# Optimization experiments

Hardware: AMD Instinct MI355X
Metric: run time of the kernel (lower is better)

The kernel has to match this reference:

```python
import jax, jax.numpy as jnp
import numpy as np

INPUT_SIZE = 768
HIDDEN = [512, 256, 128]
LATENT = 32
NUM_LEVELS = 3
CODEBOOK_SIZE = 256
BATCH = 131072


def _init_linear(key, d_in, d_out):
    kw, kb = jax.random.split(key)
    lim = 1.0 / np.sqrt(d_in)
    W = jax.random.uniform(kw, (d_in, d_out), jnp.float32, -lim, lim)
    b = jax.random.uniform(kb, (d_out,), jnp.float32, -lim, lim)
    return W, b


def setup_inputs() -> dict:
    key = jax.random.key(0)
    keys = jax.random.split(key, 16)
    inp = {"x": jax.random.normal(keys[0], (BATCH, INPUT_SIZE), jnp.float32)}
    enc_dims = [INPUT_SIZE] + HIDDEN + [LATENT]          # 768->512->256->128->32
    dec_dims = [LATENT] + HIDDEN[::-1] + [INPUT_SIZE]     # 32->128->256->512->768
    for i in range(4):
        W, b = _init_linear(keys[1 + i], enc_dims[i], enc_dims[i + 1])
        inp[f"enc_W{i}"], inp[f"enc_b{i}"] = W, b
        W, b = _init_linear(keys[6 + i], dec_dims[i], dec_dims[i + 1])
        inp[f"dec_W{i}"], inp[f"dec_b{i}"] = W, b
    inp["codebooks"] = jax.random.normal(keys[12], (NUM_LEVELS, CODEBOOK_SIZE, LATENT), jnp.float32)
    return inp


def _mlp(x, Ws, bs):
    # Linear -> ReLU (-> Dropout p=0, identity) between layers, final layer linear.
    n = len(Ws)
    for i in range(n):
        x = x @ Ws[i] + bs[i]
        if i < n - 1:
            x = jax.nn.relu(x)
    return x


def _quantize(z, codebooks):
    # Residual vector quantization over NUM_LEVELS codebooks.
    L, K, D = codebooks.shape
    r = z
    idxs, rs, es = [], [], []
    for l in range(L):
        c = codebooks[l]                                  # [K, D]
        # squared-distance argmin (same argmin as cdist)
        d = jnp.sum(r * r, axis=-1, keepdims=True) - 2.0 * (r @ c.T) + jnp.sum(c * c, axis=-1)
        idx = jnp.argmin(d, axis=-1)                      # [B]
        e = c[idx]                                        # [B, D] gather
        idxs.append(idx)
        rs.append(r)
        es.append(e)
        r = r - e
    quantized = jnp.stack(idxs, axis=1)                   # [B, L] int codes
    r_stack = jnp.stack(rs, axis=1)                       # [B, L, D] residual inputs per level
    e_stack = jnp.stack(es, axis=1)                       # [B, L, D] selected embeddings
    sum_e = jnp.sum(e_stack, axis=1)                      # [B, D]
    # straight-through estimator
    z_hat = z + jax.lax.stop_gradient(sum_e - z)
    counts = jnp.sum(jax.nn.one_hot(quantized, K, dtype=jnp.float32), axis=0)  # [L, K] usage
    return quantized, r_stack, e_stack, z_hat, counts


def reference(x,
              enc_W0, enc_b0, enc_W1, enc_b1, enc_W2, enc_b2, enc_W3, enc_b3,
              dec_W0, dec_b0, dec_W1, dec_b1, dec_W2, dec_b2, dec_W3, dec_b3,
              codebooks):
    encoded = _mlp(x, [enc_W0, enc_W1, enc_W2, enc_W3], [enc_b0, enc_b1, enc_b2, enc_b3])
    quantized, r, e, z_hat, counts = _quantize(encoded, codebooks)
    decoded = _mlp(z_hat, [dec_W0, dec_W1, dec_W2, dec_W3], [dec_b0, dec_b1, dec_b2, dec_b3])
    return decoded, r, e, counts, quantized
```

## Files before the change

### kernel.cpp

```cpp
#include <hip/hip_runtime.h>
#include <hip/hip_bf16.h>
#include <cfloat>

#define B_TOTAL 131072
#define IN_DIM  768
#define NLEV    3
#define KCODE   256

typedef unsigned short u16;
typedef unsigned int   u32;
typedef __attribute__((ext_vector_type(8))) short bf16x8;
typedef __attribute__((ext_vector_type(4))) float f32x4;

#define GLOAD_LDS(g, l)                                                        \
    __builtin_amdgcn_global_load_lds(                                          \
        (const __attribute__((address_space(1))) u32*)(g),                     \
        (__attribute__((address_space(3))) u32*)(l), 16, 0, 0)

#define SWZ(row) ((((row) >> 1) & 3u) << 4)

__device__ __forceinline__ u16 f2bf(float x) {
    union { __hip_bfloat16 h; u16 u; } c;
    c.h = __float2bfloat16(x);
    return c.u;
}
__device__ __forceinline__ float bf2f(u32 lo16) {
    union { u32 v; float f; } c;
    c.v = lo16 << 16;
    return c.f;
}
__device__ __forceinline__ u32 pack2(float a, float b) {
    return (u32)f2bf(a) | ((u32)f2bf(b) << 16);
}

__device__ __forceinline__ u32 xcd_swizzle(u32 orig, u32 nwg) {
    const u32 xcd = orig & 7u, q8 = nwg >> 3, r8 = nwg & 7u;
    return (xcd < r8 ? xcd * (q8 + 1) : r8 * (q8 + 1) + (xcd - r8) * q8)
           + (orig >> 3);
}

template<int K, int N, bool AF32, bool RELU, bool OUTF32>
__global__ __launch_bounds__(512)
void gemm_mfma(const void* __restrict__ A_, const u16* __restrict__ Wt,
               const float* __restrict__ bias, void* __restrict__ C_)
{
    constexpr int NK  = K / 32;
    constexpr int NCB = N / 128;
    __shared__ u16 As[3][8192];
    __shared__ u16 Bs[3][4096];

    const int tid  = threadIdx.x;
    const int lane = tid & 63;
    const int wid  = tid >> 6;
    const int wrow = wid >> 1;
    const int wcol = wid & 1;

    const u32 wg = xcd_swizzle(blockIdx.x, gridDim.x);
    const int col0 = (int)(wg % NCB) * 128;
    const int row0 = (int)(wg / NCB) * 256;

    const u16*   Ab = (const u16*)A_;
    const float* Af = (const float*)A_;

    f32x4 acc[4][4];
    #pragma unroll
    for (int i = 0; i < 4; ++i)
        #pragma unroll
        for (int j = 0; j < 4; ++j) acc[i][j] = (f32x4){0.f, 0.f, 0.f, 0.f};

    auto stage_B = [&](u16* dstbase, const u16* src) {
        const u32 o   = (u32)(tid * 16);
        const u32 row = o >> 6;
        const u32 cbs = (o & 63u) ^ SWZ(row);
        GLOAD_LDS((const char*)(src + (size_t)row * K) + cbs,
                  dstbase + wid * 512);
    };
    auto stage_A = [&](u16* dstbase, const u16* src) {
        #pragma unroll
        for (int i = 0; i < 2; ++i) {
            const u32 o   = (u32)(i * 8192 + tid * 16);
            const u32 row = o >> 6;
            const u32 cbs = (o & 63u) ^ SWZ(row);
            GLOAD_LDS((const char*)(src + (size_t)row * K) + cbs,
                      dstbase + (i * 4096 + wid * 512));
        }
    };
    auto stage_tile = [&](int buf, int kt) {
        stage_B(&Bs[buf][0], Wt + (size_t)col0 * K + kt * 32);
        stage_A(&As[buf][0], Ab + (size_t)row0 * K + kt * 32);
    };

    auto compute = [&](int buf) {
        const char* Ab8 = (const char*)&As[buf][0];
        const char* Bb8 = (const char*)&Bs[buf][0];
        const int kb = (lane >> 4) * 16;
        bf16x8 af[4], bf[4];
        #pragma unroll
        for (int mf = 0; mf < 4; ++mf) {
            const int r = wrow * 64 + mf * 16 + (lane & 15);
            af[mf] = *(const bf16x8*)(Ab8 + r * 64 + (kb ^ SWZ(r)));
        }
        #pragma unroll
        for (int nf = 0; nf < 4; ++nf) {
            const int r = wcol * 64 + nf * 16 + (lane & 15);
            bf[nf] = *(const bf16x8*)(Bb8 + r * 64 + (kb ^ SWZ(r)));
        }
        __builtin_amdgcn_s_setprio(1);
        #pragma unroll
        for (int mf = 0; mf < 4; ++mf)
            #pragma unroll
            for (int nf = 0; nf < 4; ++nf)
                acc[mf][nf] = __builtin_amdgcn_mfma_f32_16x16x32_bf16(
                    af[mf], bf[nf], acc[mf][nf], 0, 0, 0);
        __builtin_amdgcn_s_setprio(0);
    };

    if constexpr (AF32) {
        float4 fa[4];
        auto loadA = [&](int kt) {
            const int row = tid >> 1;
            const int ce0 = (tid & 1) * 16;
            const float* s = &Af[(size_t)(row0 + row) * K + kt * 32 + ce0];
            fa[0] = *(const float4*)(s + 0);
            fa[1] = *(const float4*)(s + 4);
            fa[2] = *(const float4*)(s + 8);
            fa[3] = *(const float4*)(s + 12);
        };
        auto writeA = [&](int buf) {
            const int row = tid >> 1;
            const u32 cb0 = (u32)((tid & 1) * 32);
            const u32 sw  = SWZ(row);
            char* lb = (char*)&As[buf][0] + row * 64;
            *(uint4*)(lb + ((cb0 + 0) ^ sw)) = make_uint4(
                pack2(fa[0].x, fa[0].y), pack2(fa[0].z, fa[0].w),
                pack2(fa[1].x, fa[1].y), pack2(fa[1].z, fa[1].w));
            *(uint4*)(lb + ((cb0 + 16) ^ sw)) = make_uint4(
                pack2(fa[2].x, fa[2].y), pack2(fa[2].z, fa[2].w),
                pack2(fa[3].x, fa[3].y), pack2(fa[3].z, fa[3].w));
        };

        loadA(0);
        stage_B(&Bs[0][0], Wt + (size_t)col0 * K);
        writeA(0);
        if (NK > 1) {
            loadA(1);
            stage_B(&Bs[1][0], Wt + (size_t)col0 * K + 32);
        }

        #pragma unroll 1
        for (int kt = 0; kt < NK; ++kt) {
            if (kt == NK - 1) asm volatile("s_waitcnt vmcnt(0) lgkmcnt(0)");
            else              asm volatile("s_waitcnt vmcnt(5) lgkmcnt(0)");
            __builtin_amdgcn_sched_barrier(0);
            __builtin_amdgcn_s_barrier();
            __builtin_amdgcn_sched_barrier(0);
            if (kt + 1 < NK) writeA((kt + 1) % 3);
            if (kt + 2 < NK) {
                loadA(kt + 2);
                stage_B(&Bs[(kt + 2) % 3][0],
                        Wt + (size_t)col0 * K + (kt + 2) * 32);
            }
            compute(kt % 3);
        }
    } else {
        stage_tile(0, 0);
        if (NK > 1) stage_tile(1, 1);
        int cb_ = 0, sb_ = 2;
        #pragma unroll 1
        for (int kt = 0; kt < NK; ++kt) {
            if (kt == NK - 1) asm volatile("s_waitcnt vmcnt(0)");
            else              asm volatile("s_waitcnt vmcnt(3)");
            __builtin_amdgcn_sched_barrier(0);
            __builtin_amdgcn_s_barrier();
            __builtin_amdgcn_sched_barrier(0);
            if (kt + 2 < NK) stage_tile(sb_, kt + 2);
            compute(cb_);
            cb_ = (cb_ == 2) ? 0 : cb_ + 1;
            sb_ = (sb_ == 2) ? 0 : sb_ + 1;
        }
    }

    #pragma unroll
    for (int nf = 0; nf < 4; ++nf) {
        const int col = col0 + wcol * 64 + nf * 16 + (lane & 15);
        const float bv = bias[col];
        #pragma unroll
        for (int mf = 0; mf < 4; ++mf) {
            const int rbase = row0 + wrow * 64 + mf * 16 + (lane >> 4) * 4;
            #pragma unroll
            for (int r = 0; r < 4; ++r) {
                float o = acc[mf][nf][r] + bv;
                if (RELU) o = fmaxf(o, 0.f);
                if constexpr (OUTF32)
                    ((float*)C_)[(size_t)(rbase + r) * N + col] = o;
                else
                    ((u16*)C_)[(size_t)(rbase + r) * N + col] = f2bf(o);
            }
        }
    }
}

__global__ __launch_bounds__(256)
void prep(const float* __restrict__ eW0, const float* __restrict__ eW1,
          const float* __restrict__ eW2, const float* __restrict__ dW0,
          const float* __restrict__ dW1, const float* __restrict__ dW2,
          const float* __restrict__ dW3,
          u16* __restrict__ tE0, u16* __restrict__ tE1, u16* __restrict__ tE2,
          u16* __restrict__ tD0, u16* __restrict__ tD1, u16* __restrict__ tD2,
          u16* __restrict__ tD3, u32* __restrict__ ghist)
{
    const int i = blockIdx.x * 256 + threadIdx.x;
    if (i < 393216) {
        const int k = i >> 9, n = i & 511;
        tE0[(size_t)n * 768 + k] = f2bf(eW0[i]);
    } else if (i < 524288) {
        const int j = i - 393216, k = j >> 8, n = j & 255;
        tE1[(size_t)n * 512 + k] = f2bf(eW1[j]);
    } else if (i < 557056) {
        const int j = i - 524288, k = j >> 7, n = j & 127;
        tE2[(size_t)n * 256 + k] = f2bf(eW2[j]);
    } else if (i < 561152) {
        const int j = i - 557056, k = j >> 7, n = j & 127;
        tD0[(size_t)n * 32 + k] = f2bf(dW0[j]);
    } else if (i < 593920) {
        const int j = i - 561152, k = j >> 8, n = j & 255;
        tD1[(size_t)n * 128 + k] = f2bf(dW1[j]);
    } else if (i < 724992) {
        const int j = i - 593920, k = j >> 9, n = j & 511;
        tD2[(size_t)n * 256 + k] = f2bf(dW2[j]);
    } else if (i < 1118208) {
        const int j = i - 724992, k = j / 768, n = j - k * 768;
        tD3[(size_t)n * 512 + k] = f2bf(dW3[j]);
    } else if (i < 1118976) {
        ghist[i - 1118208] = 0;
    }
}

__global__ __launch_bounds__(256)
void vq_kernel(const u16* __restrict__ h3, const float* __restrict__ eW3,
               const float* __restrict__ eb3, const float* __restrict__ cb,
               float* __restrict__ r_out, float* __restrict__ e_out,
               float* __restrict__ q_out, u16* __restrict__ se_ws,
               u32* __restrict__ ghist, size_t grow_base)
{
    __shared__ float W3[128 * 32];
    __shared__ float ebv[32];
    __shared__ float clds[256 * 36];
    __shared__ float cc2[256];
    __shared__ u32   lh[NLEV * KCODE];

    const int tid = threadIdx.x;
    const size_t lrow = (size_t)blockIdx.x * 256 + tid;
    const size_t grow = grow_base + lrow;

    for (int i = tid; i < 128 * 32; i += 256) W3[i] = eW3[i];
    if (tid < 32) ebv[tid] = eb3[tid];
    for (int i = tid; i < NLEV * KCODE; i += 256) lh[i] = 0;
    __syncthreads();

    float r[32];
    #pragma unroll
    for (int j = 0; j < 32; ++j) r[j] = ebv[j];
    {
        const u32* hrow = (const u32*)h3 + lrow * 64;
        #pragma unroll 2
        for (int k2 = 0; k2 < 64; ++k2) {
            const u32 v = hrow[k2];
            const float x0 = bf2f(v & 0xffffu), x1 = bf2f(v >> 16);
            const float* w0 = &W3[(2 * k2) * 32];
            const float* w1 = &W3[(2 * k2 + 1) * 32];
            #pragma unroll
            for (int j4 = 0; j4 < 8; ++j4) {
                const float4 a = *(const float4*)&w0[4 * j4];
                const float4 b = *(const float4*)&w1[4 * j4];
                r[4*j4+0] = fmaf(x1, b.x, fmaf(x0, a.x, r[4*j4+0]));
                r[4*j4+1] = fmaf(x1, b.y, fmaf(x0, a.y, r[4*j4+1]));
                r[4*j4+2] = fmaf(x1, b.z, fmaf(x0, a.z, r[4*j4+2]));
                r[4*j4+3] = fmaf(x1, b.w, fmaf(x0, a.w, r[4*j4+3]));
            }
        }
    }

    float z0[32];
    #pragma unroll
    for (int j = 0; j < 32; ++j) z0[j] = r[j];

    #pragma unroll 1
    for (int l = 0; l < NLEV; ++l) {
        __syncthreads();
        {
            const float* cl = cb + ((size_t)l * KCODE + tid) * 32;
            float s = 0.f;
            #pragma unroll
            for (int m = 0; m < 8; ++m) {
                const float4 v = *(const float4*)&cl[4 * m];
                *(float4*)&clds[tid * 36 + 4 * m] = v;
                s = fmaf(v.x, v.x, s); s = fmaf(v.y, v.y, s);
                s = fmaf(v.z, v.z, s); s = fmaf(v.w, v.w, s);
            }
            cc2[tid] = -0.5f * s;
        }
        __syncthreads();

        float best = -FLT_MAX;
        int   bidx = 0;
        #pragma unroll 1
        for (int k = 0; k < KCODE; ++k) {
            const float* ck = &clds[k * 36];
            float d0 = 0.f, d1 = 0.f, d2 = 0.f, d3 = 0.f;
            #pragma unroll
            for (int m = 0; m < 8; m += 4) {
                const float4 v0 = *(const float4*)&ck[4 * (m + 0)];
                const float4 v1 = *(const float4*)&ck[4 * (m + 1)];
                const float4 v2 = *(const float4*)&ck[4 * (m + 2)];
                const float4 v3 = *(const float4*)&ck[4 * (m + 3)];
                d0 = fmaf(r[4*m+0],  v0.x, d0); d0 = fmaf(r[4*m+1],  v0.y, d0);
                d0 = fmaf(r[4*m+2],  v0.z, d0); d0 = fmaf(r[4*m+3],  v0.w, d0);
                d1 = fmaf(r[4*m+4],  v1.x, d1); d1 = fmaf(r[4*m+5],  v1.y, d1);
                d1 = fmaf(r[4*m+6],  v1.z, d1); d1 = fmaf(r[4*m+7],  v1.w, d1);
                d2 = fmaf(r[4*m+8],  v2.x, d2); d2 = fmaf(r[4*m+9],  v2.y, d2);
                d2 = fmaf(r[4*m+10], v2.z, d2); d2 = fmaf(r[4*m+11], v2.w, d2);
                d3 = fmaf(r[4*m+12], v3.x, d3); d3 = fmaf(r[4*m+13], v3.y, d3);
                d3 = fmaf(r[4*m+14], v3.z, d3); d3 = fmaf(r[4*m+15], v3.w, d3);
            }
            const float s = ((d0 + d1) + (d2 + d3)) + cc2[k];
            if (s > best) { best = s; bidx = k; }
        }

        const size_t base = (grow * NLEV + l) * 32;
        const float* ce = &clds[bidx * 36];
        #pragma unroll
        for (int m = 0; m < 8; ++m) {
            const float4 ev = *(const float4*)&ce[4 * m];
            *(float4*)&r_out[base + 4 * m] =
                make_float4(r[4*m+0], r[4*m+1], r[4*m+2], r[4*m+3]);
            *(float4*)&e_out[base + 4 * m] = ev;
            r[4*m+0] -= ev.x; r[4*m+1] -= ev.y;
            r[4*m+2] -= ev.z; r[4*m+3] -= ev.w;
        }
        q_out[grow * NLEV + l] = (float)bidx;
        atomicAdd(&lh[l * KCODE + bidx], 1u);
    }

    u32* sed = (u32*)se_ws + lrow * 16;
    #pragma unroll
    for (int m = 0; m < 16; ++m)
        sed[m] = pack2(z0[2*m] - r[2*m], z0[2*m+1] - r[2*m+1]);

    __syncthreads();
    for (int i = tid; i < NLEV * KCODE; i += 256)
        if (lh[i]) atomicAdd(&ghist[i], lh[i]);
}

__global__ void counts_fin(const u32* __restrict__ g, float* __restrict__ o) {
    if (threadIdx.x < NLEV * KCODE) o[threadIdx.x] = (float)g[threadIdx.x];
}

__global__ __launch_bounds__(256)
void counts_k(const float* __restrict__ q, float* __restrict__ cnt)
{
    const int l = blockIdx.x >> 8;
    const int k = blockIdx.x & 255;
    const float pat = (float)k;
    int c = 0;
    for (int i = threadIdx.x; i < B_TOTAL; i += 256)
        c += (q[(size_t)i * NLEV + l] == pat) ? 1 : 0;
    __shared__ int red[256];
    red[threadIdx.x] = c;
    __syncthreads();
    for (int s = 128; s > 0; s >>= 1) {
        if (threadIdx.x < s) red[threadIdx.x] += red[threadIdx.x + s];
        __syncthreads();
    }
    if (threadIdx.x == 0)
        cnt[blockIdx.x] = (float)red[0];
}

template<int K, int N, bool RELU, bool AGLOBAL>
static __device__ __forceinline__
void layer16(const float* __restrict__ A, size_t grow0,
             const float* __restrict__ W, const float* __restrict__ bias,
             float* __restrict__ C)
{
    constexpr int QPT = N / 128;
    const int tr = threadIdx.x >> 5;
    const int tc = threadIdx.x & 31;
    float acc[2][QPT * 4];
    #pragma unroll
    for (int i = 0; i < 2; ++i)
        #pragma unroll
        for (int j = 0; j < QPT * 4; ++j) acc[i][j] = 0.f;
    #pragma unroll 2
    for (int k0 = 0; k0 < K; k0 += 4) {
        float4 av[2];
        #pragma unroll
        for (int i = 0; i < 2; ++i) {
            if (AGLOBAL)
                av[i] = *(const float4*)&A[(grow0 + tr * 2 + i) * (size_t)K + k0];
            else
                av[i] = *(const float4*)&A[(tr * 2 + i) * K + k0];
        }
        #pragma unroll
        for (int kk = 0; kk < 4; ++kk) {
            #pragma unroll
            for (int q = 0; q < QPT; ++q) {
                const float4 w4 = *(const float4*)&W[(size_t)(k0 + kk) * N + 4 * (tc + 32 * q)];
                #pragma unroll
                for (int i = 0; i < 2; ++i) {
                    const float a = ((const float*)&av[i])[kk];
                    acc[i][4*q+0] = fmaf(a, w4.x, acc[i][4*q+0]);
                    acc[i][4*q+1] = fmaf(a, w4.y, acc[i][4*q+1]);
                    acc[i][4*q+2] = fmaf(a, w4.z, acc[i][4*q+2]);
                    acc[i][4*q+3] = fmaf(a, w4.w, acc[i][4*q+3]);
                }
            }
        }
    }
    #pragma unroll
    for (int q = 0; q < QPT; ++q) {
        const float4 b4 = *(const float4*)&bias[4 * (tc + 32 * q)];
        #pragma unroll
        for (int i = 0; i < 2; ++i) {
            float4 o;
            o.x = acc[i][4*q+0] + b4.x; o.y = acc[i][4*q+1] + b4.y;
            o.z = acc[i][4*q+2] + b4.z; o.w = acc[i][4*q+3] + b4.w;
            if (RELU) {
                o.x = fmaxf(o.x, 0.f); o.y = fmaxf(o.y, 0.f);
                o.z = fmaxf(o.z, 0.f); o.w = fmaxf(o.w, 0.f);
            }
            *(float4*)&C[(tr * 2 + i) * N + 4 * (tc + 32 * q)] = o;
        }
    }
}

static __device__ __forceinline__
void layer_final16(const float* __restrict__ A, const float* __restrict__ W,
                   const float* __restrict__ bias, float* __restrict__ Cg, size_t grow0)
{
    constexpr int QPT = 6;
    const int tr = threadIdx.x >> 5;
    const int tc = threadIdx.x & 31;
    float acc[2][QPT * 4];
    #pragma unroll
    for (int i = 0; i < 2; ++i)
        #pragma unroll
        for (int j = 0; j < QPT * 4; ++j) acc[i][j] = 0.f;
    #pragma unroll 2
    for (int k0 = 0; k0 < 512; k0 += 4) {
        float4 av[2];
        #pragma unroll
        for (int i = 0; i < 2; ++i)
            av[i] = *(const float4*)&A[(tr * 2 + i) * 512 + k0];
        #pragma unroll
        for (int kk = 0; kk < 4; ++kk) {
            #pragma unroll
            for (int q = 0; q < QPT; ++q) {
                const float4 w4 = *(const float4*)&W[(size_t)(k0 + kk) * 768 + 4 * (tc + 32 * q)];
                #pragma unroll
                for (int i = 0; i < 2; ++i) {
                    const float a = ((const float*)&av[i])[kk];
                    acc[i][4*q+0] = fmaf(a, w4.x, acc[i][4*q+0]);
                    acc[i][4*q+1] = fmaf(a, w4.y, acc[i][4*q+1]);
                    acc[i][4*q+2] = fmaf(a, w4.z, acc[i][4*q+2]);
                    acc[i][4*q+3] = fmaf(a, w4.w, acc[i][4*q+3]);
                }
            }
        }
    }
    #pragma unroll
    for (int q = 0; q < QPT; ++q) {
        const float4 b4 = *(const float4*)&bias[4 * (tc + 32 * q)];
        #pragma unroll
        for (int i = 0; i < 2; ++i) {
            float4 s;
            s.x = acc[i][4*q+0] + b4.x; s.y = acc[i][4*q+1] + b4.y;
            s.z = acc[i][4*q+2] + b4.z; s.w = acc[i][4*q+3] + b4.w;
            *(float4*)&Cg[(grow0 + tr * 2 + i) * (size_t)768 + 4 * (tc + 32 * q)] = s;
        }
    }
}

static __device__ __forceinline__
void layer_narrow16(const float* __restrict__ A, const float* __restrict__ W,
                    const float* __restrict__ bias, float* __restrict__ Z)
{
    const int row = threadIdx.x >> 4;
    const int g   = threadIdx.x & 15;
    float a0 = 0.f, a1 = 0.f;
    #pragma unroll 4
    for (int k0 = 0; k0 < 128; k0 += 4) {
        const float4 av = *(const float4*)&A[row * 128 + k0];
        #pragma unroll
        for (int kk = 0; kk < 4; ++kk) {
            const float2 w2 = *(const float2*)&W[(k0 + kk) * 32 + 2 * g];
            const float a = ((const float*)&av)[kk];
            a0 = fmaf(a, w2.x, a0);
            a1 = fmaf(a, w2.y, a1);
        }
    }
    Z[row * 36 + 2 * g + 0] = a0 + bias[2 * g + 0];
    Z[row * 36 + 2 * g + 1] = a1 + bias[2 * g + 1];
}

__global__ __launch_bounds__(256)
void enc_vq_kernel(const float* __restrict__ x,
                   const float* __restrict__ eW0, const float* __restrict__ eb0,
                   const float* __restrict__ eW1, const float* __restrict__ eb1,
                   const float* __restrict__ eW2, const float* __restrict__ eb2,
                   const float* __restrict__ eW3, const float* __restrict__ eb3,
                   const float* __restrict__ cb,
                   float* __restrict__ r_out, float* __restrict__ e_out,
                   float* __restrict__ q_out)
{
    __shared__ __align__(16) char smem[59648];
    float* h1   = (float*)(smem);
    float* h2   = (float*)(smem + 32768);
    float* h3   = (float*)(smem + 49152);
    float* z    = (float*)(smem + 57344);
    float* clds = (float*)(smem);
    float* cc   = (float*)(smem + 36864);

    const size_t grow0 = (size_t)blockIdx.x * 16;
    layer16<768, 512, true, true >(x,  grow0, eW0, eb0, h1);
    __syncthreads();
    layer16<512, 256, true, false>(h1, 0,     eW1, eb1, h2);
    __syncthreads();
    layer16<256, 128, true, false>(h2, 0,     eW2, eb2, h3);
    __syncthreads();
    layer_narrow16(h3, eW3, eb3, z);

    const int row = threadIdx.x >> 4;
    const int g   = threadIdx.x & 15;
    const size_t grow = grow0 + row;

    #pragma unroll 1
    for (int l = 0; l < NLEV; ++l) {
        __syncthreads();
        {
            const float* cl = cb + (size_t)l * KCODE * 32;
            const int t = threadIdx.x;
            float s = 0.f;
            #pragma unroll
            for (int m = 0; m < 8; ++m) {
                const float4 v = *(const float4*)&cl[t * 32 + 4 * m];
                *(float4*)&clds[t * 36 + 4 * m] = v;
                s = fmaf(v.x, v.x, s); s = fmaf(v.y, v.y, s);
                s = fmaf(v.z, v.z, s); s = fmaf(v.w, v.w, s);
            }
            cc[t] = s;
        }
        __syncthreads();

        float r[32];
        #pragma unroll
        for (int m = 0; m < 8; ++m) {
            const float4 v = *(const float4*)&z[row * 36 + 4 * m];
            r[4*m+0] = v.x; r[4*m+1] = v.y; r[4*m+2] = v.z; r[4*m+3] = v.w;
        }
        float rr = 0.f;
        #pragma unroll
        for (int j = 0; j < 32; ++j) rr = fmaf(r[j], r[j], rr);

        float best = FLT_MAX;
        int   bidx = 0x7fffffff;
        #pragma unroll 1
        for (int t = 0; t < 16; ++t) {
            const int k = g + 16 * t;
            const float* ck = &clds[k * 36];
            float d0 = 0.f, d1 = 0.f, d2 = 0.f, d3 = 0.f;
            #pragma unroll
            for (int m = 0; m < 8; m += 4) {
                const float4 v0 = *(const float4*)&ck[4 * (m + 0)];
                const float4 v1 = *(const float4*)&ck[4 * (m + 1)];
                const float4 v2 = *(const float4*)&ck[4 * (m + 2)];
                const float4 v3 = *(const float4*)&ck[4 * (m + 3)];
                d0 = fmaf(r[4*m+0],  v0.x, d0); d0 = fmaf(r[4*m+1],  v0.y, d0);
                d0 = fmaf(r[4*m+2],  v0.z, d0); d0 = fmaf(r[4*m+3],  v0.w, d0);
                d1 = fmaf(r[4*m+4],  v1.x, d1); d1 = fmaf(r[4*m+5],  v1.y, d1);
                d1 = fmaf(r[4*m+6],  v1.z, d1); d1 = fmaf(r[4*m+7],  v1.w, d1);
                d2 = fmaf(r[4*m+8],  v2.x, d2); d2 = fmaf(r[4*m+9],  v2.y, d2);
                d2 = fmaf(r[4*m+10], v2.z, d2); d2 = fmaf(r[4*m+11], v2.w, d2);
                d3 = fmaf(r[4*m+12], v3.x, d3); d3 = fmaf(r[4*m+13], v3.y, d3);
                d3 = fmaf(r[4*m+14], v3.z, d3); d3 = fmaf(r[4*m+15], v3.w, d3);
            }
            const float dot = (d0 + d1) + (d2 + d3);
            const float d = (rr - 2.f * dot) + cc[k];
            if (d < best || (d == best && k < bidx)) { best = d; bidx = k; }
        }
        #pragma unroll
        for (int off = 1; off < 16; off <<= 1) {
            const float ob = __shfl_xor(best, off);
            const int   oi = __shfl_xor(bidx, off);
            if (ob < best || (ob == best && oi < bidx)) { best = ob; bidx = oi; }
        }

        const float evx = clds[bidx * 36 + 2 * g + 0];
        const float evy = clds[bidx * 36 + 2 * g + 1];
        *(float2*)&r_out[(grow * NLEV + l) * 32 + 2 * g] = make_float2(r[2*g], r[2*g+1]);
        *(float2*)&e_out[(grow * NLEV + l) * 32 + 2 * g] = make_float2(evx, evy);
        if (g == 0) q_out[grow * NLEV + l] = (float)bidx;
        z[row * 36 + 2 * g + 0] = r[2 * g + 0] - evx;
        z[row * 36 + 2 * g + 1] = r[2 * g + 1] - evy;
    }
}

__global__ __launch_bounds__(256)
void dec_kernel(const float* __restrict__ e_in,
                const float* __restrict__ dW0, const float* __restrict__ db0,
                const float* __restrict__ dW1, const float* __restrict__ db1,
                const float* __restrict__ dW2, const float* __restrict__ db2,
                const float* __restrict__ dW3, const float* __restrict__ db3,
                float* __restrict__ dec_out)
{
    __shared__ __align__(16) char smem[59392];
    float* h3 = (float*)(smem);
    float* h2 = (float*)(smem + 32768);
    float* h1 = (float*)(smem + 49152);
    float* se = (float*)(smem + 57344);

    const size_t grow0 = (size_t)blockIdx.x * 16;
    const int row = threadIdx.x >> 4;
    const int g   = threadIdx.x & 15;
    {
        const size_t base = ((grow0 + row) * NLEV) * 32 + 2 * g;
        float s0 = 0.f, s1 = 0.f;
        #pragma unroll
        for (int l = 0; l < NLEV; ++l) {
            const float2 v = *(const float2*)&e_in[base + l * 32];
            s0 += v.x; s1 += v.y;
        }
        se[row * 32 + 2 * g + 0] = s0;
        se[row * 32 + 2 * g + 1] = s1;
    }
    __syncthreads();
    layer16<32,  128, true, false>(se, 0, dW0, db0, h1);
    __syncthreads();
    layer16<128, 256, true, false>(h1, 0, dW1, db1, h2);
    __syncthreads();
    layer16<256, 512, true, false>(h2, 0, dW2, db2, h3);
    __syncthreads();
    layer_final16(h3, dW3, db3, dec_out, grow0);
}

extern "C" void kernel_launch(void* const* d_in, const int* in_sizes, int n_in,
                              void* d_out, int out_size, void* d_ws, size_t ws_size,
                              hipStream_t stream)
{
    (void)in_sizes; (void)n_in; (void)out_size;
    const float* x  = (const float*)d_in[0];
    const float* cb = (const float*)d_in[17];
    const float *eW[4], *eb[4], *dW[4], *db[4];
    for (int i = 0; i < 4; ++i) {
        eW[i] = (const float*)d_in[1 + 4 * i];
        eb[i] = (const float*)d_in[2 + 4 * i];
        dW[i] = (const float*)d_in[3 + 4 * i];
        db[i] = (const float*)d_in[4 + 4 * i];
    }

    float* out = (float*)d_out;
    const size_t OFF_R = (size_t)B_TOTAL * IN_DIM;
    const size_t OFF_E = OFF_R + (size_t)B_TOTAL * NLEV * 32;
    const size_t OFF_C = OFF_E + (size_t)B_TOTAL * NLEV * 32;
    const size_t OFF_Q = OFF_C + (size_t)NLEV * KCODE;

    const size_t WTB = 2236416;
    size_t R = 0;
    for (size_t cand = 131072; cand >= 2048; cand >>= 1)
        if (WTB + cand * 3648 + 4096 <= ws_size) { R = cand; break; }

    if (R && d_ws) {
        u16* Wp   = (u16*)d_ws;
        u16* WtE0 = Wp;
        u16* WtE1 = WtE0 + 393216;
        u16* WtE2 = WtE1 + 131072;
        u16* WtD0 = WtE2 + 32768;
        u16* WtD1 = WtD0 + 4096;
        u16* WtD2 = WtD1 + 32768;
        u16* WtD3 = WtD2 + 131072;
        u16* h1   = WtD3 + 393216;
        u16* h2   = h1 + R * 512;
        u16* h3   = h2 + R * 256;
        u16* se   = h3 + R * 128;
        u16* d1   = se + R * 32;
        u16* d2   = d1 + R * 128;
        u16* d3   = d2 + R * 256;
        u32* ghist = (u32*)(d3 + R * 512);

        prep<<<dim3(4371), 256, 0, stream>>>(
            eW[0], eW[1], eW[2], dW[0], dW[1], dW[2], dW[3],
            WtE0, WtE1, WtE2, WtD0, WtD1, WtD2, WtD3, ghist);

        const int nch = B_TOTAL / (int)R;
        const int MB2 = (int)R / 256;
        for (int c = 0; c < nch; ++c) {
            const size_t rb = (size_t)c * R;
            gemm_mfma<768, 512, true,  true,  false><<<dim3(4 * MB2), 512, 0, stream>>>(
                x + rb * 768, WtE0, eb[0], h1);
            gemm_mfma<512, 256, false, true,  false><<<dim3(2 * MB2), 512, 0, stream>>>(
                h1, WtE1, eb[1], h2);
            gemm_mfma<256, 128, false, true,  false><<<dim3(1 * MB2), 512, 0, stream>>>(
                h2, WtE2, eb[2], h3);
            vq_kernel<<<dim3((int)R / 256), 256, 0, stream>>>(
                h3, eW[3], eb[3], cb,
                out + OFF_R, out + OFF_E, out + OFF_Q, se, ghist, rb);
            gemm_mfma<32,  128, false, true,  false><<<dim3(1 * MB2), 512, 0, stream>>>(
                se, WtD0, db[0], d1);
            gemm_mfma<128, 256, false, true,  false><<<dim3(2 * MB2), 512, 0, stream>>>(
                d1, WtD1, db[1], d2);
            gemm_mfma<256, 512, false, true,  false><<<dim3(4 * MB2), 512, 0, stream>>>(
                d2, WtD2, db[2], d3);
            gemm_mfma<512, 768, false, false, true ><<<dim3(6 * MB2), 512, 0, stream>>>(
                d3, WtD3, db[3], out + rb * 768);
        }
        counts_fin<<<1, 768, 0, stream>>>(ghist, out + OFF_C);
    } else {
        enc_vq_kernel<<<dim3(B_TOTAL / 16), 256, 0, stream>>>(
            x, eW[0], eb[0], eW[1], eb[1], eW[2], eb[2], eW[3], eb[3], cb,
            out + OFF_R, out + OFF_E, out + OFF_Q);
        counts_k<<<dim3(NLEV * KCODE), 256, 0, stream>>>(out + OFF_Q, out + OFF_C);
        dec_kernel<<<dim3(B_TOTAL / 16), 256, 0, stream>>>(
            out + OFF_E, dW[0], db[0], dW[1], db[1], dW[2], db[2], dW[3], db[3], out);
    }
}
```

Baseline: 837.9 us.

## Fuse first decoder layer into VQ kernel and double its block size

The first decoder linear layer (32->128 with ReLU) now runs inside the VQ kernel in scalar FP32 FMAs, reusing the shared weight buffer after quantization. This removes one GEMM launch and the write and re-read of the sum-of-embeddings intermediate. The VQ kernel also moves to 512 threads per block, so the codebook staging in LDS is shared across more rows. In exchange, each thread does 4096 extra scalar FMAs instead of MFMA work, and the larger block may hurt occupancy and raise register pressure.

Measured after the change: 856.8 us. 2.3% more time.

```diff
diff --git a/kernel.cpp b/kernel.cpp
--- a/kernel.cpp
+++ b/kernel.cpp
@@ -236,26 +236,29 @@
     }
 }
 
-__global__ __launch_bounds__(256)
+__global__ __launch_bounds__(512)
 void vq_kernel(const u16* __restrict__ h3, const float* __restrict__ eW3,
                const float* __restrict__ eb3, const float* __restrict__ cb,
+               const float* __restrict__ dW0, const float* __restrict__ db0,
                float* __restrict__ r_out, float* __restrict__ e_out,
-               float* __restrict__ q_out, u16* __restrict__ se_ws,
+               float* __restrict__ q_out, u16* __restrict__ d1_out,
                u32* __restrict__ ghist, size_t grow_base)
 {
-    __shared__ float W3[128 * 32];
+    __shared__ float Wb[128 * 32];
     __shared__ float ebv[32];
+    __shared__ float dbv[128];
     __shared__ float clds[256 * 36];
     __shared__ float cc2[256];
     __shared__ u32   lh[NLEV * KCODE];
 
     const int tid = threadIdx.x;
-    const size_t lrow = (size_t)blockIdx.x * 256 + tid;
+    const size_t lrow = (size_t)blockIdx.x * 512 + tid;
     const size_t grow = grow_base + lrow;
 
-    for (int i = tid; i < 128 * 32; i += 256) W3[i] = eW3[i];
-    if (tid < 32) ebv[tid] = eb3[tid];
-    for (int i = tid; i < NLEV * KCODE; i += 256) lh[i] = 0;
+    for (int i = tid; i < 128 * 32; i += 512) Wb[i] = eW3[i];
+    if (tid < 32)  ebv[tid] = eb3[tid];
+    if (tid < 128) dbv[tid] = db0[tid];
+    for (int i = tid; i < NLEV * KCODE; i += 512) lh[i] = 0;
     __syncthreads();
 
     float r[32];
@@ -267,8 +270,8 @@
         for (int k2 = 0; k2 < 64; ++k2) {
             const u32 v = hrow[k2];
             const float x0 = bf2f(v & 0xffffu), x1 = bf2f(v >> 16);
-            const float* w0 = &W3[(2 * k2) * 32];
-            const float* w1 = &W3[(2 * k2 + 1) * 32];
+            const float* w0 = &Wb[(2 * k2) * 32];
+            const float* w1 = &Wb[(2 * k2 + 1) * 32];
             #pragma unroll
             for (int j4 = 0; j4 < 8; ++j4) {
                 const float4 a = *(const float4*)&w0[4 * j4];
@@ -288,7 +291,7 @@
     #pragma unroll 1
     for (int l = 0; l < NLEV; ++l) {
         __syncthreads();
-        {
+        if (tid < KCODE) {
             const float* cl = cb + ((size_t)l * KCODE + tid) * 32;
             float s = 0.f;
             #pragma unroll
@@ -342,13 +345,33 @@
         atomicAdd(&lh[l * KCODE + bidx], 1u);
     }
 
-    u32* sed = (u32*)se_ws + lrow * 16;
-    #pragma unroll
-    for (int m = 0; m < 16; ++m)
-        sed[m] = pack2(z0[2*m] - r[2*m], z0[2*m+1] - r[2*m+1]);
-
-    __syncthreads();
-    for (int i = tid; i < NLEV * KCODE; i += 256)
+    __syncthreads();
+    for (int i = tid; i < 128 * 32; i += 512) Wb[i] = dW0[i];
+    __syncthreads();
+
+    float se[32];
+    #pragma unroll
+    for (int j = 0; j < 32; ++j) se[j] = z0[j] - r[j];
+
+    u16* drow = d1_out + lrow * 128;
+    #pragma unroll 2
+    for (int q4 = 0; q4 < 32; ++q4) {
+        float4 a = *(const float4*)&dbv[4 * q4];
+        #pragma unroll
+        for (int k = 0; k < 32; ++k) {
+            const float4 w = *(const float4*)&Wb[k * 128 + 4 * q4];
+            a.x = fmaf(se[k], w.x, a.x);
+            a.y = fmaf(se[k], w.y, a.y);
+            a.z = fmaf(se[k], w.z, a.z);
+            a.w = fmaf(se[k], w.w, a.w);
+        }
+        a.x = fmaxf(a.x, 0.f); a.y = fmaxf(a.y, 0.f);
+        a.z = fmaxf(a.z, 0.f); a.w = fmaxf(a.w, 0.f);
+        *(uint2*)&drow[4 * q4] = make_uint2(pack2(a.x, a.y), pack2(a.z, a.w));
+    }
+
+    __syncthreads();
+    for (int i = tid; i < NLEV * KCODE; i += 512)
         if (lh[i]) atomicAdd(&ghist[i], lh[i]);
 }
 
@@ -680,8 +703,7 @@
         u16* h1   = WtD3 + 393216;
         u16* h2   = h1 + R * 512;
         u16* h3   = h2 + R * 256;
-        u16* se   = h3 + R * 128;
-        u16* d1   = se + R * 32;
+        u16* d1   = h3 + R * 128;
         u16* d2   = d1 + R * 128;
         u16* d3   = d2 + R * 256;
         u32* ghist = (u32*)(d3 + R * 512);
@@ -700,11 +722,9 @@
                 h1, WtE1, eb[1], h2);
             gemm_mfma<256, 128, false, true,  false><<<dim3(1 * MB2), 512, 0, stream>>>(
                 h2, WtE2, eb[2], h3);
-            vq_kernel<<<dim3((int)R / 256), 256, 0, stream>>>(
-                h3, eW[3], eb[3], cb,
-                out + OFF_R, out + OFF_E, out + OFF_Q, se, ghist, rb);
-            gemm_mfma<32,  128, false, true,  false><<<dim3(1 * MB2), 512, 0, stream>>>(
-                se, WtD0, db[0], d1);
+            vq_kernel<<<dim3((int)R / 512), 512, 0, stream>>>(
+                h3, eW[3], eb[3], cb, dW[0], db[0],
+                out + OFF_R, out + OFF_E, out + OFF_Q, d1, ghist, rb);
             gemm_mfma<128, 256, false, true,  false><<<dim3(2 * MB2), 512, 0, stream>>>(
                 d1, WtD1, db[1], d2);
             gemm_mfma<256, 512, false, true,  false><<<dim3(4 * MB2), 512, 0, stream>>>(
```
